# Performance work log

Hardware: AMD Instinct MI355X
Metric: run time of the kernel (lower is better)

## Reference

```python
import jax, jax.numpy as jnp
import numpy as np

K = 3
PAD = 1


def conv3x3(x, w):
    # x: [B,C,H,W], w: [O,C,3,3] -> [B,O,H,W], stride 1, pad 1, no bias
    return jax.lax.conv_general_dilated(
        x, w, window_strides=(1, 1), padding=((PAD, PAD), (PAD, PAD)),
        dimension_numbers=("NCHW", "OIHW", "NCHW"))


def bilinear_gather(x, py, px):
    """Zero-padded bilinear sampling (torchvision deform_conv2d semantics).
    x: [B,C,H,W]; py, px: [B,KK,H,W] absolute sampling coords.
    Returns [B,C,KK,H,W]."""
    B, C, H, W = x.shape
    KK = py.shape[1]
    y0 = jnp.floor(py)
    x0 = jnp.floor(px)
    wy1 = py - y0  # frac weights
    wx1 = px - x0
    wy0 = 1.0 - wy1
    wx0 = 1.0 - wx1
    x_flat = x.reshape(B, C, H * W)

    def corner(yi, xi, w):
        valid = (yi >= 0) & (yi <= H - 1) & (xi >= 0) & (xi <= W - 1)
        yc = jnp.clip(yi, 0, H - 1).astype(jnp.int32)
        xc = jnp.clip(xi, 0, W - 1).astype(jnp.int32)
        idx = (yc * W + xc).reshape(B, 1, KK * H * W)
        v = jnp.take_along_axis(x_flat, jnp.broadcast_to(idx, (B, C, KK * H * W)), axis=2)
        v = v.reshape(B, C, KK, H, W)
        return v * (w * valid.astype(x.dtype))[:, None]

    return (corner(y0, x0, wy0 * wx0) + corner(y0, x0 + 1.0, wy0 * wx1)
            + corner(y0 + 1.0, x0, wy1 * wx0) + corner(y0 + 1.0, x0 + 1.0, wy1 * wx1))


def deform_conv2d(x, offset, weight):
    """x: [B,C,H,W]; offset: [B,2*K*K,H,W] (dy,dx interleaved per tap, row-major);
    weight: [O,C,K,K]. stride 1, pad 1, dilation 1, 1 group, 1 offset group."""
    B, C, H, W = x.shape
    O = weight.shape[0]
    off = offset.reshape(B, K * K, 2, H, W)
    dy, dx = off[:, :, 0], off[:, :, 1]  # [B,9,H,W]
    ki, kj = jnp.meshgrid(jnp.arange(K, dtype=x.dtype), jnp.arange(K, dtype=x.dtype), indexing="ij")
    ki = ki.reshape(1, K * K, 1, 1)
    kj = kj.reshape(1, K * K, 1, 1)
    hh = jnp.arange(H, dtype=x.dtype).reshape(1, 1, H, 1)
    ww = jnp.arange(W, dtype=x.dtype).reshape(1, 1, 1, W)
    py = hh - PAD + ki + dy  # [B,9,H,W]
    px = ww - PAD + kj + dx
    sampled = bilinear_gather(x, py, px)  # [B,C,9,H,W]
    return jnp.einsum("bckhw,ock->bohw", sampled, weight.reshape(O, C, K * K))


def offset_estimator(x, w1, w2, w3):
    # channel-preserving bottleneck stand-in for Dynamic_offset_estimator
    h = jax.nn.relu(conv3x3(x, w1))
    h = jax.nn.relu(conv3x3(h, w2))
    return conv3x3(h, w3)


def setup_inputs() -> dict:
    key = jax.random.key(0)
    ks = jax.random.split(key, 7)
    B, C, H, W = 1, 768, 64, 64
    C2, CM = 2 * C, 192
    f32 = jnp.float32
    inp = {
        "input_features": jax.random.normal(ks[0], (B, C, H, W), dtype=f32),
        "reference_features": jax.random.normal(ks[1], (B, C, H, W), dtype=f32),
        "est_w1": jax.random.normal(ks[2], (CM, C2, K, K), dtype=f32) / np.sqrt(C2 * K * K),
        "est_w2": jax.random.normal(ks[3], (CM, CM, K, K), dtype=f32) / np.sqrt(CM * K * K),
        "est_w3": jax.random.normal(ks[4], (C2, CM, K, K), dtype=f32) / np.sqrt(CM * K * K),
        "offset_w": jax.random.normal(ks[5], (18, C2, K, K), dtype=f32) / np.sqrt(C2 * K * K),
        "deform_w": jax.random.normal(ks[6], (C, C, K, K), dtype=f32) / np.sqrt(C * K * K),
    }
    return inp


def reference(input_features, reference_features, est_w1, est_w2, est_w3, offset_w, deform_w):
    input_offset = jnp.concatenate([input_features, reference_features], axis=1)  # [B,2C,H,W]
    est = offset_estimator(input_offset, est_w1, est_w2, est_w3)  # [B,2C,H,W]
    offset = conv3x3(est, offset_w)  # [B,18,H,W]
    return deform_conv2d(reference_features, offset, deform_w)  # [B,C,H,W]
```

## Files before the change

### kernel.cpp

```cpp
#include <hip/hip_runtime.h>

#define HWPX 4096

typedef short s8v  __attribute__((ext_vector_type(8)));
typedef float f4v  __attribute__((ext_vector_type(4)));

__device__ inline unsigned short f2bf(float f) {
    unsigned u = __float_as_uint(f);
    return (unsigned short)((u + 0x7fffu + ((u >> 16) & 1u)) >> 16);
}
__device__ inline float bf2f(unsigned s) {
    return __uint_as_float(s << 16);
}

__global__ __launch_bounds__(256)
void tr_cat_k(const float* __restrict__ xa, const float* __restrict__ xb,
              short* __restrict__ xt)
{
    __shared__ __align__(16) short T[64 * 72];
    const int c0 = blockIdx.x * 64, p0 = blockIdx.y * 64, tid = threadIdx.x;
    for (int i = tid; i < 4096; i += 256) {
        int cl = i >> 6, pl = i & 63;
        int c = c0 + cl;
        float v = (c < 768) ? xa[(size_t)c * HWPX + p0 + pl]
                            : xb[(size_t)(c - 768) * HWPX + p0 + pl];
        T[pl * 72 + cl] = (short)f2bf(v);
    }
    __syncthreads();
    for (int i = tid; i < 512; i += 256) {
        int pl = i >> 3, part = i & 7;
        uint4 v = *(const uint4*)&T[pl * 72 + part * 8];
        *(uint4*)&xt[(size_t)(p0 + pl) * 1536 + c0 + part * 8] = v;
    }
}

__device__ inline void wpack1(const float* __restrict__ src, short* __restrict__ dst,
                              int i, int Cin, int Cout, int S, int NB)
{
    int e = i & 7, lane = (i >> 3) & 63;
    int lm = lane & 15, quad = lane >> 4;
    int rest = i >> 9;
    int f = rest % NB;
    int s = (rest / NB) % S;
    int g = rest / (NB * S);
    int cout = g * (NB * 16) + f * 16 + lm;
    int cb = s / 9, t = s % 9;
    int ch = cb * 32 + quad * 8 + e;
    dst[i] = (cout < Cout) ? (short)f2bf(src[((size_t)cout * Cin + ch) * 9 + t]) : 0;
}

#define C1 2654208
#define C2 2985984
#define C3 5640192
#define C4 6082560
#define C5 11390976

__global__ __launch_bounds__(256)
void wpack_all_k(const float* __restrict__ s1, const float* __restrict__ s2,
                 const float* __restrict__ s3, const float* __restrict__ s4,
                 const float* __restrict__ s5,
                 short* __restrict__ d1, short* __restrict__ d2,
                 short* __restrict__ d3, short* __restrict__ d4,
                 short* __restrict__ d5)
{
    int i = blockIdx.x * 256 + threadIdx.x;
    if (i < C1)      wpack1(s1, d1, i,      1536, 192,  432, 4);
    else if (i < C2) wpack1(s2, d2, i - C1, 192,  192,  54,  4);
    else if (i < C3) wpack1(s3, d3, i - C2, 192,  1536, 54,  4);
    else if (i < C4) wpack1(s4, d4, i - C3, 1536, 18,   432, 2);
    else if (i < C5) wpack1(s5, d5, i - C4, 768,  768,  216, 4);
}

template<int NB>
__global__ __launch_bounds__(256, 3)
void convf_k(const short* __restrict__ Xt, int CinStr,
             const short* __restrict__ Wp, int S, int chunks,
             short* __restrict__ Out, int Cstr, int splitStride)
{
    __shared__ __align__(16) short sH[6 * 66 * 40];
    const int tid = threadIdx.x, lane = tid & 63, wv = tid >> 6;
    const int lm = lane & 15, quad = lane >> 4;
    const int r0 = blockIdx.x * 4;
    const int g  = blockIdx.y;
    const int cb0 = blockIdx.z * chunks;
    short* out = Out + (size_t)blockIdx.z * splitStride;

    f4v acc[4][NB];
#pragma unroll
    for (int ma = 0; ma < 4; ++ma)
#pragma unroll
        for (int nb = 0; nb < NB; ++nb)
#pragma unroll
            for (int r = 0; r < 4; ++r) acc[ma][nb][r] = 0.f;

    for (int cc = 0; cc < chunks; ++cc) {
        const int cb = cb0 + cc;
        const short* wpB = Wp + ((size_t)(g * S + cb * 9) * NB) * 512 + lane * 8;
        s8v bb[NB];
#pragma unroll
        for (int f = 0; f < NB; ++f)
            bb[f] = *(const s8v*)&wpB[(size_t)f * 512];

        for (int i = tid; i < 1584; i += 256) {
            int slot = i >> 2, part = i & 3;
            int hr = slot / 66, px = slot % 66;
            int gy = r0 - 1 + hr, gx = px - 1;
            uint4 v = {0, 0, 0, 0};
            if (gy >= 0 && gy < 64 && gx >= 0 && gx < 64)
                v = *(const uint4*)&Xt[(size_t)(gy * 64 + gx) * CinStr + cb * 32 + part * 8];
            *(uint4*)&sH[slot * 40 + part * 8] = v;
        }
        __syncthreads();

#pragma unroll
        for (int t = 0; t < 9; ++t) {
            const int ty = t / 3, tx = t % 3;
            s8v nxt[NB];
#pragma unroll
            for (int f = 0; f < NB; ++f)
                nxt[f] = *(const s8v*)&wpB[(size_t)((t + 1) * NB + f) * 512];
            s8v a[4];
#pragma unroll
            for (int ma = 0; ma < 4; ++ma)
                a[ma] = *(const s8v*)&sH[((wv + ty) * 66 + ma * 16 + lm + tx) * 40 + quad * 8];
#pragma unroll
            for (int ma = 0; ma < 4; ++ma)
#pragma unroll
                for (int nb = 0; nb < NB; ++nb)
                    acc[ma][nb] = __builtin_amdgcn_mfma_f32_16x16x32_bf16(
                        a[ma], bb[nb], acc[ma][nb], 0, 0, 0);
#pragma unroll
            for (int f = 0; f < NB; ++f) bb[f] = nxt[f];
        }
        __syncthreads();
    }

    const int py = (r0 + wv) * 64;
#pragma unroll
    for (int ma = 0; ma < 4; ++ma)
#pragma unroll
        for (int nb = 0; nb < NB; ++nb)
#pragma unroll
            for (int r = 0; r < 4; ++r)
                out[(size_t)(py + ma * 16 + quad * 4 + r) * Cstr
                    + g * (NB * 16) + nb * 16 + lm] = (short)f2bf(acc[ma][nb][r]);
}

__global__ __launch_bounds__(256)
void ep_sumb_k(const short* __restrict__ P, short* __restrict__ outb,
               int nsplit, size_t splitStride, int n8, int relu)
{
    int i = blockIdx.x * 256 + threadIdx.x;
    if (i >= n8) return;
    size_t base = (size_t)i * 8;
    float s[8];
#pragma unroll
    for (int j = 0; j < 8; ++j) s[j] = 0.f;
    for (int sp = 0; sp < nsplit; ++sp) {
        uint4 v = *(const uint4*)&P[sp * splitStride + base];
        s[0] += bf2f(v.x & 0xffffu); s[1] += bf2f(v.x >> 16);
        s[2] += bf2f(v.y & 0xffffu); s[3] += bf2f(v.y >> 16);
        s[4] += bf2f(v.z & 0xffffu); s[5] += bf2f(v.z >> 16);
        s[6] += bf2f(v.w & 0xffffu); s[7] += bf2f(v.w >> 16);
    }
    if (relu) {
#pragma unroll
        for (int j = 0; j < 8; ++j) s[j] = fmaxf(s[j], 0.f);
    }
    uint4 o;
    o.x = f2bf(s[0]) | ((unsigned)f2bf(s[1]) << 16);
    o.y = f2bf(s[2]) | ((unsigned)f2bf(s[3]) << 16);
    o.z = f2bf(s[4]) | ((unsigned)f2bf(s[5]) << 16);
    o.w = f2bf(s[6]) | ((unsigned)f2bf(s[7]) << 16);
    *(uint4*)&outb[base] = o;
}

__global__ __launch_bounds__(256)
void ep_offs_k(const short* __restrict__ P, float* __restrict__ offs, int nsplit)
{
    int i = blockIdx.x * 256 + threadIdx.x;
    if (i >= 18 * HWPX) return;
    int m = i >> 12, px = i & 4095;
    float s = 0.f;
    for (int sp = 0; sp < nsplit; ++sp)
        s += bf2f((unsigned short)P[((size_t)sp * HWPX + px) * 32 + m]);
    offs[i] = s;
}

__global__ __launch_bounds__(256)
void sample_k(const short* __restrict__ xcat, const float* __restrict__ offs,
              short* __restrict__ Smp)
{
    __shared__ int   s_mi[9][16][4];
    __shared__ float s_mw[9][16][4];
    const int tid = threadIdx.x;
    const int p0  = blockIdx.x * 16;
    const int gb  = blockIdx.y * 24;

    if (tid < 144) {
        int t = tid / 16, p = tid % 16;
        int pxg = p0 + p;
        int r = pxg >> 6, x = pxg & 63;
        float dy = offs[(size_t)(2 * t)     * HWPX + pxg];
        float dx = offs[(size_t)(2 * t + 1) * HWPX + pxg];
        float py  = (float)(r - 1 + t / 3) + dy;
        float pxf = (float)(x - 1 + t % 3) + dx;
        py  = fminf(fmaxf(py,  -1e6f), 1e6f);
        pxf = fminf(fmaxf(pxf, -1e6f), 1e6f);
        float y0f = floorf(py), x0f = floorf(pxf);
        float wy1 = py - y0f, wx1 = pxf - x0f;
        float wy0 = 1.f - wy1, wx0 = 1.f - wx1;
        bool vy0 = (y0f >=  0.f) && (y0f <= 63.f);
        bool vy1 = (y0f >= -1.f) && (y0f <= 62.f);
        bool vx0 = (x0f >=  0.f) && (x0f <= 63.f);
        bool vx1 = (x0f >= -1.f) && (x0f <= 62.f);
        int y0 = (int)fminf(fmaxf(y0f,       0.f), 63.f);
        int y1 = (int)fminf(fmaxf(y0f + 1.f, 0.f), 63.f);
        int x0 = (int)fminf(fmaxf(x0f,       0.f), 63.f);
        int x1 = (int)fminf(fmaxf(x0f + 1.f, 0.f), 63.f);
        s_mi[t][p][0] = y0 * 64 + x0;  s_mw[t][p][0] = (vy0 && vx0) ? wy0 * wx0 : 0.f;
        s_mi[t][p][1] = y0 * 64 + x1;  s_mw[t][p][1] = (vy0 && vx1) ? wy0 * wx1 : 0.f;
        s_mi[t][p][2] = y1 * 64 + x0;  s_mw[t][p][2] = (vy1 && vx0) ? wy1 * wx0 : 0.f;
        s_mi[t][p][3] = y1 * 64 + x1;  s_mw[t][p][3] = (vy1 && vx1) ? wy1 * wx1 : 0.f;
    }
    __syncthreads();

    for (int i = tid; i < 16 * 9 * 24; i += 256) {
        int p = i / 216, rest = i % 216;
        int t = rest / 24, g = gb + rest % 24;
        float a[8];
#pragma unroll
        for (int j = 0; j < 8; ++j) a[j] = 0.f;
#pragma unroll
        for (int c = 0; c < 4; ++c) {
            float w = s_mw[t][p][c];
            const short* src = xcat + (size_t)s_mi[t][p][c] * 1536 + 768 + g * 8;
            uint4 v = *(const uint4*)src;
            a[0] += w * bf2f(v.x & 0xffffu); a[1] += w * bf2f(v.x >> 16);
            a[2] += w * bf2f(v.y & 0xffffu); a[3] += w * bf2f(v.y >> 16);
            a[4] += w * bf2f(v.z & 0xffffu); a[5] += w * bf2f(v.z >> 16);
            a[6] += w * bf2f(v.w & 0xffffu); a[7] += w * bf2f(v.w >> 16);
        }
        uint4 o;
        o.x = f2bf(a[0]) | ((unsigned)f2bf(a[1]) << 16);
        o.y = f2bf(a[2]) | ((unsigned)f2bf(a[3]) << 16);
        o.z = f2bf(a[4]) | ((unsigned)f2bf(a[5]) << 16);
        o.w = f2bf(a[6]) | ((unsigned)f2bf(a[7]) << 16);
        int px = p0 + p;
        int pg = px >> 6, ma = (px >> 4) & 3, lmx = px & 15;
        int cb = g >> 2, qd = g & 3;
        size_t addr = ((((size_t)pg * 216 + cb * 9 + t) * 4 + ma) * 64 + qd * 16 + lmx) * 8;
        *(uint4*)&Smp[addr] = o;
    }
}

__global__ __launch_bounds__(256, 3)
void dgemm_k(const short* __restrict__ Ap, const short* __restrict__ Bp,
             short* __restrict__ P)
{
    const int tid = threadIdx.x, lane = tid & 63, wv = tid >> 6;
    const int lm = lane & 15, quad = lane >> 4;
    const int mg = blockIdx.y * 2 + (wv >> 1);
    const int pg = blockIdx.x * 2 + (wv & 1);
    const int s0 = blockIdx.z * 54;
    const short* ap = Ap + (((size_t)mg * 216 + s0) * 4 * 64 + lane) * 8;
    const short* bp = Bp + (((size_t)pg * 216 + s0) * 4 * 64 + lane) * 8;

    f4v acc[4][4];
#pragma unroll
    for (int ma = 0; ma < 4; ++ma)
#pragma unroll
        for (int nb = 0; nb < 4; ++nb)
#pragma unroll
            for (int r = 0; r < 4; ++r) acc[ma][nb][r] = 0.f;

    s8v a0[4], b0[4], a1[4], b1[4];
#pragma unroll
    for (int f = 0; f < 4; ++f) {
        a0[f] = *(const s8v*)&ap[(size_t)f * 512];
        b0[f] = *(const s8v*)&bp[(size_t)f * 512];
    }

    for (int s = 0; s < 54; s += 2) {
#pragma unroll
        for (int f = 0; f < 4; ++f) {
            a1[f] = *(const s8v*)&ap[(size_t)((s + 1) * 4 + f) * 512];
            b1[f] = *(const s8v*)&bp[(size_t)((s + 1) * 4 + f) * 512];
        }
#pragma unroll
        for (int ma = 0; ma < 4; ++ma)
#pragma unroll
            for (int nb = 0; nb < 4; ++nb)
                acc[ma][nb] = __builtin_amdgcn_mfma_f32_16x16x32_bf16(
                    a0[ma], b0[nb], acc[ma][nb], 0, 0, 0);
#pragma unroll
        for (int f = 0; f < 4; ++f) {
            a0[f] = *(const s8v*)&ap[(size_t)((s + 2) * 4 + f) * 512];
            b0[f] = *(const s8v*)&bp[(size_t)((s + 2) * 4 + f) * 512];
        }
#pragma unroll
        for (int ma = 0; ma < 4; ++ma)
#pragma unroll
            for (int nb = 0; nb < 4; ++nb)
                acc[ma][nb] = __builtin_amdgcn_mfma_f32_16x16x32_bf16(
                    a1[ma], b1[nb], acc[ma][nb], 0, 0, 0);
    }

    short* p = P + (size_t)blockIdx.z * 768 * HWPX;
#pragma unroll
    for (int ma = 0; ma < 4; ++ma)
#pragma unroll
        for (int nb = 0; nb < 4; ++nb)
#pragma unroll
            for (int r = 0; r < 4; ++r)
                p[(size_t)(mg * 64 + ma * 16 + quad * 4 + r) * HWPX
                  + pg * 64 + nb * 16 + lm] = (short)f2bf(acc[ma][nb][r]);
}

__global__ __launch_bounds__(256)
void ep_dg_k(const short* __restrict__ P, float* __restrict__ out)
{
    int i = blockIdx.x * 256 + threadIdx.x;
    if (i >= 768 * HWPX / 8) return;
    size_t base = (size_t)i * 8;
    float s[8];
#pragma unroll
    for (int j = 0; j < 8; ++j) s[j] = 0.f;
    for (int sp = 0; sp < 4; ++sp) {
        uint4 v = *(const uint4*)&P[(size_t)sp * 768 * HWPX + base];
        s[0] += bf2f(v.x & 0xffffu); s[1] += bf2f(v.x >> 16);
        s[2] += bf2f(v.y & 0xffffu); s[3] += bf2f(v.y >> 16);
        s[4] += bf2f(v.z & 0xffffu); s[5] += bf2f(v.z >> 16);
        s[6] += bf2f(v.w & 0xffffu); s[7] += bf2f(v.w >> 16);
    }
    float4 o0 = make_float4(s[0], s[1], s[2], s[3]);
    float4 o1 = make_float4(s[4], s[5], s[6], s[7]);
    *(float4*)&out[base]     = o0;
    *(float4*)&out[base + 4] = o1;
}

extern "C" void kernel_launch(void* const* d_in, const int* in_sizes, int n_in,
                              void* d_out, int out_size, void* d_ws, size_t ws_size,
                              hipStream_t stream)
{
    const float* x_in  = (const float*)d_in[0];
    const float* x_ref = (const float*)d_in[1];
    const float* w1    = (const float*)d_in[2];
    const float* w2    = (const float*)d_in[3];
    const float* w3    = (const float*)d_in[4];
    const float* ow    = (const float*)d_in[5];
    const float* dw    = (const float*)d_in[6];
    float* out = (float*)d_out;

    char* w = (char*)d_ws;
    size_t off = 0;
    auto carve = [&](size_t bytes) {
        void* p = w + off;
        off += (bytes + 255) & ~(size_t)255;
        return p;
    };
    short* xcat = (short*)carve((size_t)4096 * 1536 * 2);
    short* w1p  = (short*)carve((size_t)C1 * 2);
    short* w2p  = (short*)carve((size_t)(C2 - C1) * 2);
    short* w3p  = (short*)carve((size_t)(C3 - C2) * 2);
    short* w4p  = (short*)carve((size_t)(C4 - C3) * 2);
    short* dwp  = (short*)carve((size_t)(C5 - C4) * 2);
    float* offs = (float*)carve((size_t)18 * 4096 * 4);
    short* Smp  = (short*)carve((size_t)4096 * 6912 * 2);
    char*  R    = (char*)carve((size_t)2 * 768 * 4096 * 4);
    short* rh1  = (short*)R;
    short* rh2  = (short*)(R + 1572864);
    short* est  = (short*)(R + 3145728);
    short* Pcv  = Smp;
    short* Pdg  = (short*)R;

    tr_cat_k<<<dim3(24, 64), 256, 0, stream>>>(x_in, x_ref, xcat);
    wpack_all_k<<<(C5 + 255) / 256, 256, 0, stream>>>(w1, w2, w3, ow, dw,
                                                      w1p, w2p, w3p, w4p, dwp);

    const int n8 = 4096 * 192 / 8;
    convf_k<4><<<dim3(16, 3, 16), 256, 0, stream>>>(xcat, 1536, w1p, 432, 3,
                                                    Pcv, 192, 4096 * 192);
    ep_sumb_k<<<(n8 + 255) / 256, 256, 0, stream>>>(Pcv, rh1, 16, (size_t)4096 * 192, n8, 1);
    convf_k<4><<<dim3(16, 3, 6), 256, 0, stream>>>(rh1, 192, w2p, 54, 1,
                                                   Pcv, 192, 4096 * 192);
    ep_sumb_k<<<(n8 + 255) / 256, 256, 0, stream>>>(Pcv, rh2, 6, (size_t)4096 * 192, n8, 1);
    convf_k<4><<<dim3(16, 24, 2), 256, 0, stream>>>(rh2, 192, w3p, 54, 3,
                                                    Pcv, 1536, 4096 * 1536);
    {
        const int n8c3 = 4096 * 1536 / 8;
        ep_sumb_k<<<(n8c3 + 255) / 256, 256, 0, stream>>>(Pcv, est, 2, (size_t)4096 * 1536, n8c3, 0);
    }
    convf_k<2><<<dim3(16, 1, 48), 256, 0, stream>>>(est, 1536, w4p, 432, 1,
                                                    Pcv, 32, 4096 * 32);
    ep_offs_k<<<(18 * HWPX + 255) / 256, 256, 0, stream>>>(Pcv, offs, 48);
    sample_k<<<dim3(256, 4), 256, 0, stream>>>(xcat, offs, Smp);
    dgemm_k<<<dim3(32, 6, 4), 256, 0, stream>>>(dwp, Smp, Pdg);
    ep_dg_k<<<(768 * HWPX / 8 + 255) / 256, 256, 0, stream>>>(Pdg, out);
}
```

Measured before the change: 349.2 us.

## Stage deform GEMM operands through LDS with async global-to-LDS triple buffering

The deform-conv GEMM kernel previously had each wave load its A and B fragments straight from global memory into registers. Each block has two A and two B column groups, so pairs of waves fetched the same tiles twice. Now each wave async-copies one quarter of the block's tile into a three-stage LDS ring using global_load_lds, and every wave reads its fragments back from LDS. The intent is to halve redundant global traffic and overlap the fetch two steps ahead with the MFMAs, at the cost of 48KB of LDS per block, which may cut occupancy below the 3-blocks launch bound, plus a barrier every step.

```diff
diff --git a/kernel.cpp b/kernel.cpp
--- a/kernel.cpp
+++ b/kernel.cpp
@@ -12,6 +12,11 @@
 __device__ inline float bf2f(unsigned s) {
     return __uint_as_float(s << 16);
 }
+
+#define GLDS16(gsrc, ldst) \
+    __builtin_amdgcn_global_load_lds( \
+        (const __attribute__((address_space(1))) unsigned int*)(gsrc), \
+        (__attribute__((address_space(3))) unsigned int*)(ldst), 16, 0, 0)
 
 __global__ __launch_bounds__(256)
 void tr_cat_k(const float* __restrict__ xa, const float* __restrict__ xb,
@@ -258,13 +263,23 @@
 void dgemm_k(const short* __restrict__ Ap, const short* __restrict__ Bp,
              short* __restrict__ P)
 {
+    __shared__ __align__(16) short sL[3 * 8192];
+
     const int tid = threadIdx.x, lane = tid & 63, wv = tid >> 6;
     const int lm = lane & 15, quad = lane >> 4;
     const int mg = blockIdx.y * 2 + (wv >> 1);
     const int pg = blockIdx.x * 2 + (wv & 1);
     const int s0 = blockIdx.z * 54;
-    const short* ap = Ap + (((size_t)mg * 216 + s0) * 4 * 64 + lane) * 8;
-    const short* bp = Bp + (((size_t)pg * 216 + s0) * 4 * 64 + lane) * 8;
+
+    const short* stSrc;
+    int stChunk;
+    if (wv < 2) {
+        stSrc = Ap + ((size_t)(blockIdx.y * 2 + wv) * 216 + s0) * 2048;
+        stChunk = wv * 2048;
+    } else {
+        stSrc = Bp + ((size_t)(blockIdx.x * 2 + (wv - 2)) * 216 + s0) * 2048;
+        stChunk = 4096 + (wv - 2) * 2048;
+    }
 
     f4v acc[4][4];
 #pragma unroll
@@ -274,36 +289,50 @@
 #pragma unroll
             for (int r = 0; r < 4; ++r) acc[ma][nb][r] = 0.f;
 
-    s8v a0[4], b0[4], a1[4], b1[4];
-#pragma unroll
-    for (int f = 0; f < 4; ++f) {
-        a0[f] = *(const s8v*)&ap[(size_t)f * 512];
-        b0[f] = *(const s8v*)&bp[(size_t)f * 512];
-    }
-
-    for (int s = 0; s < 54; s += 2) {
+#pragma unroll
+    for (int j = 0; j < 4; ++j)
+        GLDS16(stSrc + (size_t)0 * 2048 + j * 512 + lane * 8,
+               &sL[0 * 8192 + stChunk + j * 512]);
+#pragma unroll
+    for (int j = 0; j < 4; ++j)
+        GLDS16(stSrc + (size_t)1 * 2048 + j * 512 + lane * 8,
+               &sL[1 * 8192 + stChunk + j * 512]);
+    asm volatile("s_waitcnt vmcnt(4)" ::: "memory");
+
+    int c0 = 0, c1 = 1, c2 = 2;
+    const int aOff = (wv >> 1) * 2048;
+    const int bOff = 4096 + (wv & 1) * 2048;
+
+    for (int s = 0; s < 54; ++s) {
+        __builtin_amdgcn_s_barrier();
+        __builtin_amdgcn_sched_barrier(0);
+
+        s8v av[4], bv[4];
+        const int base = c0 * 8192;
 #pragma unroll
         for (int f = 0; f < 4; ++f) {
-            a1[f] = *(const s8v*)&ap[(size_t)((s + 1) * 4 + f) * 512];
-            b1[f] = *(const s8v*)&bp[(size_t)((s + 1) * 4 + f) * 512];
+            av[f] = *(const s8v*)&sL[base + aOff + f * 512 + lane * 8];
+            bv[f] = *(const s8v*)&sL[base + bOff + f * 512 + lane * 8];
         }
+
+        if (s < 52) {
+#pragma unroll
+            for (int j = 0; j < 4; ++j)
+                GLDS16(stSrc + (size_t)(s + 2) * 2048 + j * 512 + lane * 8,
+                       &sL[c2 * 8192 + stChunk + j * 512]);
+        }
+
 #pragma unroll
         for (int ma = 0; ma < 4; ++ma)
 #pragma unroll
             for (int nb = 0; nb < 4; ++nb)
                 acc[ma][nb] = __builtin_amdgcn_mfma_f32_16x16x32_bf16(
-                    a0[ma], b0[nb], acc[ma][nb], 0, 0, 0);
-#pragma unroll
-        for (int f = 0; f < 4; ++f) {
-            a0[f] = *(const s8v*)&ap[(size_t)((s + 2) * 4 + f) * 512];
-            b0[f] = *(const s8v*)&bp[(size_t)((s + 2) * 4 + f) * 512];
-        }
-#pragma unroll
-        for (int ma = 0; ma < 4; ++ma)
-#pragma unroll
-            for (int nb = 0; nb < 4; ++nb)
-                acc[ma][nb] = __builtin_amdgcn_mfma_f32_16x16x32_bf16(
-                    a1[ma], b1[nb], acc[ma][nb], 0, 0, 0);
+                    av[ma], bv[nb], acc[ma][nb], 0, 0, 0);
+
+        if (s < 52) asm volatile("s_waitcnt vmcnt(4)" ::: "memory");
+        else        asm volatile("s_waitcnt vmcnt(0)" ::: "memory");
+
+        int t = c0; c0 = c1; c1 = c2; c2 = t;
     }
 
     short* p = P + (size_t)blockIdx.z * 768 * HWPX;
```

Result: no change. 342.5 us (-1.9%).
